# Kernel tuning notes

Hardware: AMD Instinct MI355X
Metric: run time of the kernel (lower is better)

## Reference

```python
import jax, jax.numpy as jnp
import numpy as np

B, D, R, NOBJ = 131072, 128, 2, 9

def setup_inputs() -> dict:
    key = jax.random.key(0)
    k1, k2, k3, k4, k5, k6 = jax.random.split(key, 6)
    return {
        "img": jax.random.normal(k1, (B, 4), dtype=jnp.float32),
        "random_int": jax.random.randint(k2, (B,), 0, NOBJ),
        "normal_sample": jax.random.normal(k3, (B, D), dtype=jnp.float32),
        "orthogonal_set": jax.random.normal(k4, (D, D), dtype=jnp.float32),
        "mu_": jax.random.uniform(k5, (NOBJ, D), dtype=jnp.float32),
        "var_": jax.random.uniform(k6, (NOBJ, R), dtype=jnp.float32),
    }

def reference(img, random_int, normal_sample, orthogonal_set, mu_, var_):
    # one_hot @ mu_ / var_ is a gather over the objective axis
    principle_mean = mu_[random_int]          # [B, D]
    principle_var = var_[random_int]          # [B, R]
    # transformer = ortho @ diag(pad(var^2)); only first R diagonal entries
    # are nonzero, so transformer @ z == ortho[:, :R] @ (var^2 * z[:, :R])
    scaled = jnp.square(principle_var) * normal_sample[:, :R]   # [B, R]
    normal_embedding = jnp.einsum('dr,br->bd', orthogonal_set[:, :R], scaled) + principle_mean
    return normal_embedding
```

## Files before the change

kernel.cpp:

```cpp
#include <hip/hip_runtime.h>
#include <hip/hip_bf16.h>


#define VAE_D 128

typedef float f32x4 __attribute__((ext_vector_type(4)));

__global__ __launch_bounds__(256)
void vae_embed_kernel(const int* __restrict__ idx,
                      const float* __restrict__ ns,
                      const float* __restrict__ ortho,
                      const float* __restrict__ mu,
                      const float* __restrict__ var,
                      float* __restrict__ out,
                      int B)
{
    const int t    = threadIdx.x;
    const int lane = t & 31;
    const int grp  = t >> 5;
    const int d0   = lane << 2;

    const float2 oc0 = *reinterpret_cast<const float2*>(ortho + (size_t)(d0 + 0) * VAE_D);
    const float2 oc1 = *reinterpret_cast<const float2*>(ortho + (size_t)(d0 + 1) * VAE_D);
    const float2 oc2 = *reinterpret_cast<const float2*>(ortho + (size_t)(d0 + 2) * VAE_D);
    const float2 oc3 = *reinterpret_cast<const float2*>(ortho + (size_t)(d0 + 3) * VAE_D);

    const int groups = B >> 3;
    const int g0 = blockIdx.x * 8;

    if (g0 + 8 <= groups) {
        int    o[8];
        float2 n[8];

        #pragma unroll
        for (int u = 0; u < 8; ++u) {
            const int b = ((g0 + u) << 3) + grp;
            o[u] = idx[b];
        }
        #pragma unroll
        for (int u = 0; u < 8; ++u) {
            const int b = ((g0 + u) << 3) + grp;
            n[u] = *reinterpret_cast<const float2*>(ns + (size_t)b * VAE_D);
        }
        #pragma unroll
        for (int u = 0; u < 8; ++u) {
            const int b = ((g0 + u) << 3) + grp;
            const float2 v = *reinterpret_cast<const float2*>(var + o[u] * 2);
            const float a0 = v.x * v.x * n[u].x;
            const float a1 = v.y * v.y * n[u].y;
            const float4 m = *reinterpret_cast<const float4*>(mu + (size_t)o[u] * VAE_D + d0);
            f32x4 r;
            r.x = fmaf(oc0.x, a0, fmaf(oc0.y, a1, m.x));
            r.y = fmaf(oc1.x, a0, fmaf(oc1.y, a1, m.y));
            r.z = fmaf(oc2.x, a0, fmaf(oc2.y, a1, m.z));
            r.w = fmaf(oc3.x, a0, fmaf(oc3.y, a1, m.w));
            __builtin_nontemporal_store(r,
                reinterpret_cast<f32x4*>(out + (size_t)b * VAE_D + d0));
        }
    } else {
        for (int g = g0; g < groups; ++g) {
            const int b = (g << 3) + grp;
            const int o = idx[b];
            const float2 n01 = *reinterpret_cast<const float2*>(ns + (size_t)b * VAE_D);
            const float2 v   = *reinterpret_cast<const float2*>(var + o * 2);
            const float a0 = v.x * v.x * n01.x;
            const float a1 = v.y * v.y * n01.y;
            const float4 m = *reinterpret_cast<const float4*>(mu + (size_t)o * VAE_D + d0);
            float4 r;
            r.x = fmaf(oc0.x, a0, fmaf(oc0.y, a1, m.x));
            r.y = fmaf(oc1.x, a0, fmaf(oc1.y, a1, m.y));
            r.z = fmaf(oc2.x, a0, fmaf(oc2.y, a1, m.z));
            r.w = fmaf(oc3.x, a0, fmaf(oc3.y, a1, m.w));
            *reinterpret_cast<float4*>(out + (size_t)b * VAE_D + d0) = r;
        }
    }
}

extern "C" void kernel_launch(void* const* d_in, const int* in_sizes, int n_in,
                              void* d_out, int out_size, void* d_ws, size_t ws_size,
                              hipStream_t stream)
{
    const int*   idx   = (const int*)  d_in[1];
    const float* ns    = (const float*)d_in[2];
    const float* ortho = (const float*)d_in[3];
    const float* mu    = (const float*)d_in[4];
    const float* var   = (const float*)d_in[5];
    float* out = (float*)d_out;

    const int B = in_sizes[1];
    const int groups = B >> 3;
    const int grid = (groups + 7) / 8;

    vae_embed_kernel<<<grid, 256, 0, stream>>>(idx, ns, ortho, mu, var, out, B);
}
```

Measured before the change: 19.97 us.

## Process four chunks per block with double-buffered index and noise loads

Each block now covers 32 row-groups instead of 8, split into four chunks of 8. The idx and noise loads for the next chunk are issued before the current chunk's gathers and stores, using two register buffers (software pipelining). This aims to hide global-load latency and amortize the per-block ortho loads, at the cost of a quarter as many blocks and more registers per thread.

```diff
diff --git a/kernel.cpp b/kernel.cpp
--- a/kernel.cpp
+++ b/kernel.cpp
@@ -3,8 +3,52 @@
 
 
 #define VAE_D 128
+#define CH    8
+#define NCH   4
 
 typedef float f32x4 __attribute__((ext_vector_type(4)));
+
+__device__ __forceinline__ void load_chunk(const int* __restrict__ idx,
+                                           const float* __restrict__ ns,
+                                           int gbase, int grp,
+                                           int* o, float2* n)
+{
+    #pragma unroll
+    for (int u = 0; u < CH; ++u) {
+        const int b = ((gbase + u) << 3) + grp;
+        o[u] = idx[b];
+    }
+    #pragma unroll
+    for (int u = 0; u < CH; ++u) {
+        const int b = ((gbase + u) << 3) + grp;
+        n[u] = *reinterpret_cast<const float2*>(ns + (size_t)b * VAE_D);
+    }
+}
+
+__device__ __forceinline__ void proc_chunk(const float* __restrict__ mu,
+                                           const float* __restrict__ var,
+                                           float* __restrict__ out,
+                                           int gbase, int grp, int d0,
+                                           const float2& oc0, const float2& oc1,
+                                           const float2& oc2, const float2& oc3,
+                                           const int* o, const float2* n)
+{
+    #pragma unroll
+    for (int u = 0; u < CH; ++u) {
+        const int b = ((gbase + u) << 3) + grp;
+        const float2 v = *reinterpret_cast<const float2*>(var + o[u] * 2);
+        const float a0 = v.x * v.x * n[u].x;
+        const float a1 = v.y * v.y * n[u].y;
+        const float4 m = *reinterpret_cast<const float4*>(mu + (size_t)o[u] * VAE_D + d0);
+        f32x4 r;
+        r.x = fmaf(oc0.x, a0, fmaf(oc0.y, a1, m.x));
+        r.y = fmaf(oc1.x, a0, fmaf(oc1.y, a1, m.y));
+        r.z = fmaf(oc2.x, a0, fmaf(oc2.y, a1, m.z));
+        r.w = fmaf(oc3.x, a0, fmaf(oc3.y, a1, m.w));
+        __builtin_nontemporal_store(r,
+            reinterpret_cast<f32x4*>(out + (size_t)b * VAE_D + d0));
+    }
+}
 
 __global__ __launch_bounds__(256)
 void vae_embed_kernel(const int* __restrict__ idx,
@@ -26,37 +70,24 @@
     const float2 oc3 = *reinterpret_cast<const float2*>(ortho + (size_t)(d0 + 3) * VAE_D);
 
     const int groups = B >> 3;
-    const int g0 = blockIdx.x * 8;
+    const int g0 = blockIdx.x * (CH * NCH);
 
-    if (g0 + 8 <= groups) {
-        int    o[8];
-        float2 n[8];
+    if (g0 + CH * NCH <= groups) {
+        int    oA[CH], oB[CH];
+        float2 nA[CH], nB[CH];
 
-        #pragma unroll
-        for (int u = 0; u < 8; ++u) {
-            const int b = ((g0 + u) << 3) + grp;
-            o[u] = idx[b];
-        }
-        #pragma unroll
-        for (int u = 0; u < 8; ++u) {
-            const int b = ((g0 + u) << 3) + grp;
-            n[u] = *reinterpret_cast<const float2*>(ns + (size_t)b * VAE_D);
-        }
-        #pragma unroll
-        for (int u = 0; u < 8; ++u) {
-            const int b = ((g0 + u) << 3) + grp;
-            const float2 v = *reinterpret_cast<const float2*>(var + o[u] * 2);
-            const float a0 = v.x * v.x * n[u].x;
-            const float a1 = v.y * v.y * n[u].y;
-            const float4 m = *reinterpret_cast<const float4*>(mu + (size_t)o[u] * VAE_D + d0);
-            f32x4 r;
-            r.x = fmaf(oc0.x, a0, fmaf(oc0.y, a1, m.x));
-            r.y = fmaf(oc1.x, a0, fmaf(oc1.y, a1, m.y));
-            r.z = fmaf(oc2.x, a0, fmaf(oc2.y, a1, m.z));
-            r.w = fmaf(oc3.x, a0, fmaf(oc3.y, a1, m.w));
-            __builtin_nontemporal_store(r,
-                reinterpret_cast<f32x4*>(out + (size_t)b * VAE_D + d0));
-        }
+        load_chunk(idx, ns, g0 + 0 * CH, grp, oA, nA);
+
+        load_chunk(idx, ns, g0 + 1 * CH, grp, oB, nB);
+        proc_chunk(mu, var, out, g0 + 0 * CH, grp, d0, oc0, oc1, oc2, oc3, oA, nA);
+
+        load_chunk(idx, ns, g0 + 2 * CH, grp, oA, nA);
+        proc_chunk(mu, var, out, g0 + 1 * CH, grp, d0, oc0, oc1, oc2, oc3, oB, nB);
+
+        load_chunk(idx, ns, g0 + 3 * CH, grp, oB, nB);
+        proc_chunk(mu, var, out, g0 + 2 * CH, grp, d0, oc0, oc1, oc2, oc3, oA, nA);
+
+        proc_chunk(mu, var, out, g0 + 3 * CH, grp, d0, oc0, oc1, oc2, oc3, oB, nB);
     } else {
         for (int g = g0; g < groups; ++g) {
             const int b = (g << 3) + grp;
@@ -89,7 +120,7 @@
 
     const int B = in_sizes[1];
     const int groups = B >> 3;
-    const int grid = (groups + 7) / 8;
+    const int grid = (groups + CH * NCH - 1) / (CH * NCH);
 
     vae_embed_kernel<<<grid, 256, 0, stream>>>(idx, ns, ortho, mu, var, out, B);
 }
```

Result: faster. 18.78 us (-6.0%).
